# Kernel optimization log

Hardware: AMD Instinct MI355X
Metric: run time of the kernel (lower is better)

Reference implementation:

```python
import jax, jax.numpy as jnp
import numpy as np

STRIDES = {"p3": 8, "p4": 16, "p5": 32}
SHAPES = {"p3": (100, 152), "p4": (50, 76), "p5": (25, 38)}
STRIDE_SCALE = 4
ASPECT_RATIOS = (0.5, 1.0, 2.0)
SCALE_CLAMP = float(np.log(224.0 / 8.0))
TOPK = 2000


def fpn_location_coords(level):
    H, W = SHAPES[level]
    s = STRIDES[level]
    # NOTE: original code uses arange(feat_shape[2]) for x and feat_shape[3] for y,
    # with meshgrid(y_vals, x_vals); replicate exactly.
    x_vals = s * (jnp.arange(H, dtype=jnp.float32) + 0.5)
    y_vals = s * (jnp.arange(W, dtype=jnp.float32) + 0.5)
    y_grid, x_grid = jnp.meshgrid(y_vals, x_vals, indexing="ij")
    return jnp.stack([x_grid.reshape(-1), y_grid.reshape(-1)], axis=1)  # (H*W, 2)


def generate_anchors(locations, level):
    s = STRIDES[level]
    anchor_size = STRIDE_SCALE * s
    area = float(anchor_size) ** 2
    boxes = []
    for ar in ASPECT_RATIOS:
        w = (area / ar) ** 0.5
        h = area / w
        half = jnp.array([w, h], dtype=jnp.float32) * 0.5
        tl = locations - half
        br = locations + half
        boxes.append(jnp.concatenate([tl, br], axis=1))  # (HW, 4)
    boxes = jnp.stack(boxes, axis=1)  # (HW, A, 4)
    return boxes.reshape(-1, 4)


def apply_deltas(deltas, anchors):
    d = deltas
    dxy = d[:, :2]
    dwh = jnp.minimum(d[:, 2:], SCALE_CLAMP)
    centers = jnp.stack([(anchors[:, 0] + anchors[:, 2]) * 0.5,
                         (anchors[:, 1] + anchors[:, 3]) * 0.5], axis=1)
    dims = jnp.stack([anchors[:, 2] - anchors[:, 0],
                      anchors[:, 3] - anchors[:, 1]], axis=1)
    new_c = centers + dims * dxy
    new_d = dims * jnp.exp(dwh)
    return jnp.concatenate([new_c - 0.5 * new_d, new_c + 0.5 * new_d], axis=1)


def iou(b1, b2):
    # b1: (M,4), b2: (N,4) -> (M,N)
    xl = jnp.maximum(b1[:, None, 0], b2[None, :, 0])
    yl = jnp.maximum(b1[:, None, 1], b2[None, :, 1])
    xr = jnp.minimum(b1[:, None, 2], b2[None, :, 2])
    yr = jnp.minimum(b1[:, None, 3], b2[None, :, 3])
    inter = jnp.clip(xr - xl, 0.0) * jnp.clip(yr - yl, 0.0)
    a1 = (b1[:, 2] - b1[:, 0]) * (b1[:, 3] - b1[:, 1])
    a2 = (b2[:, 2] - b2[:, 0]) * (b2[:, 3] - b2[:, 1])
    return inter / (a1[:, None] + a2[None, :] - inter)


def setup_inputs() -> dict:
    key = jax.random.key(0)
    ks = jax.random.split(key, 6)
    d = {}
    d["feat_p3"] = jax.random.normal(ks[0], (1, 256, 100, 152), jnp.float32)
    d["feat_p4"] = jax.random.normal(ks[1], (1, 256, 50, 76), jnp.float32)
    d["feat_p5"] = jax.random.normal(ks[2], (1, 256, 25, 38), jnp.float32)
    d["deltas_p3"] = jax.random.normal(ks[3], (45600, 4), jnp.float32) * 0.1
    d["deltas_p4"] = jax.random.normal(ks[4], (11400, 4), jnp.float32) * 0.1
    d["deltas_p5"] = jax.random.normal(ks[5], (2850, 4), jnp.float32) * 0.1
    return d


def reference(feat_p3, feat_p4, feat_p5, deltas_p3, deltas_p4, deltas_p5):
    deltas = {"p3": deltas_p3, "p4": deltas_p4, "p5": deltas_p5}
    boxes_all = []
    anchors_all = []
    for level in ("p3", "p4", "p5"):
        locs = fpn_location_coords(level)
        anchors = generate_anchors(locs, level)
        boxes = apply_deltas(deltas[level], anchors)
        boxes_all.append(boxes)
        anchors_all.append(anchors)
    boxes = jnp.concatenate(boxes_all, axis=0)      # (59850, 4)
    anchors = jnp.concatenate(anchors_all, axis=0)  # (59850, 4)
    # proposal scoring proxy: score by box area magnitude of first TOPK slice
    proposals = boxes[:TOPK]
    ious = iou(proposals, anchors)  # (2000, 59850)
    max_iou = jnp.max(ious, axis=0)  # (59850,)
    return boxes, anchors, max_iou


if __name__ == "__main__":
    out = reference(**setup_inputs())
    print([o.shape for o in out])
```

## Files before the change

kernel.cpp:

```cpp
#include <hip/hip_runtime.h>
#include <math.h>

#define NTOT      59850
#define NPROP     2000
#define ANCH_OFF  239400
#define MIOU_OFF  478800
#define NCHUNK    32
#define CS        64
#define GXI       16
#define BUILD_PER 120

struct BuildConsts {
    float hw[3][3];
    float hh[3][3];
    float clampv;
};

__device__ __forceinline__ float4 make_box(float x, float y, float hwv, float hhv,
                                           float4 d, float clampv)
{
    float ax0 = x - hwv, ay0 = y - hhv;
    float ax1 = x + hwv, ay1 = y + hhv;
    float w  = ax1 - ax0, h = ay1 - ay0;
    float cx = (ax0 + ax1) * 0.5f, cy = (ay0 + ay1) * 0.5f;
    float dwx = fminf(d.z, clampv), dwy = fminf(d.w, clampv);
    float ncx = cx + w * d.x, ncy = cy + h * d.y;
    float nw  = w * expf(dwx), nh = h * expf(dwy);
    return make_float4(ncx - 0.5f * nw, ncy - 0.5f * nh,
                       ncx + 0.5f * nw, ncy + 0.5f * nh);
}

__device__ __forceinline__ void anchor_from_id(int g, const BuildConsts& C,
    float& x, float& y, float& hwv, float& hhv)
{
    if (g < 45600) {
        int loc = g / 3, r = g - loc * 3;
        int i = loc / 100, j = loc - i * 100;
        x = 8.f * ((float)j + 0.5f);  y = 8.f * ((float)i + 0.5f);
        hwv = C.hw[0][r]; hhv = C.hh[0][r];
    } else if (g < 57000) {
        int a = g - 45600;
        int loc = a / 3, r = a - loc * 3;
        int i = loc / 50, j = loc - i * 50;
        x = 16.f * ((float)j + 0.5f); y = 16.f * ((float)i + 0.5f);
        hwv = C.hw[1][r]; hhv = C.hh[1][r];
    } else {
        int a = g - 57000;
        int loc = a / 3, r = a - loc * 3;
        int i = loc / 25, j = loc - i * 25;
        x = 32.f * ((float)j + 0.5f); y = 32.f * ((float)i + 0.5f);
        hwv = C.hw[2][r]; hhv = C.hh[2][r];
    }
}

#define RECT(L, S, NX, NY, i0v, j0v, njv, nv)                                  \
    int i0v, j0v, njv, nv;                                                     \
    {                                                                          \
        float hwm = C.hw[L][0], hhm = C.hh[L][2];                              \
        int j0t = (int)floorf((bb.x - hwm) * (1.0f / S) - 0.5f) - 1;           \
        int j1t = (int)ceilf ((bb.z + hwm) * (1.0f / S) - 0.5f) + 1;           \
        int i0t = (int)floorf((bb.y - hhm) * (1.0f / S) - 0.5f) - 1;           \
        int i1t = (int)ceilf ((bb.w + hhm) * (1.0f / S) - 0.5f) + 1;           \
        j0t = max(0, j0t); j1t = min(NX - 1, j1t);                             \
        i0t = max(0, i0t); i1t = min(NY - 1, i1t);                             \
        int njt = j1t - j0t + 1, nit = i1t - i0t + 1;                          \
        if (njt < 0) njt = 0;                                                  \
        if (nit < 0) nit = 0;                                                  \
        i0v = i0t; j0v = j0t; njv = njt; nv = nit * njt * 3;                   \
    }

__global__ __launch_bounds__(256) void rpn_kernel(
    const float4* __restrict__ d3,
    const float4* __restrict__ d4,
    const float4* __restrict__ d5,
    float* __restrict__ out,
    BuildConsts C)
{
    __shared__ float4 Pb[CS];
    __shared__ float  Pa[CS];
    __shared__ float4 bbS;

    int tid = threadIdx.x;
    int bx  = blockIdx.x;
    int cy  = blockIdx.y;
    float* miou = out + MIOU_OFF;

    int gb = (cy * GXI + bx) * BUILD_PER + tid;
    if (tid < BUILD_PER && gb < NTOT) {
        const float4* dl; int a;
        if (gb < 45600)      { dl = d3; a = gb; }
        else if (gb < 57000) { dl = d4; a = gb - 45600; }
        else                 { dl = d5; a = gb - 57000; }
        float x, y, hwv, hhv;
        anchor_from_id(gb, C, x, y, hwv, hhv);
        ((float4*)out)[gb] = make_box(x, y, hwv, hhv, dl[a], C.clampv);
        ((float4*)(out + ANCH_OFF))[gb] =
            make_float4(x - hwv, y - hhv, x + hwv, y + hhv);
        if (((const int*)miou)[gb] < 0)
            atomicMax((int*)(miou + gb), 0);
    }

    if (tid < CS) {
        int p = cy * CS + tid;
        p = p < NPROP ? p : NPROP - 1;
        int loc = p / 3, r = p - loc * 3;
        int i = loc / 100, j = loc - i * 100;
        float x = 8.0f * ((float)j + 0.5f);
        float y = 8.0f * ((float)i + 0.5f);
        float4 b = make_box(x, y, C.hw[0][r], C.hh[0][r], d3[p], C.clampv);
        Pb[tid] = b;
        Pa[tid] = (b.z - b.x) * (b.w - b.y);
        float bx0 = b.x, by0 = b.y, bx1 = b.z, by1 = b.w;
        #pragma unroll
        for (int m = 32; m; m >>= 1) {
            bx0 = fminf(bx0, __shfl_xor(bx0, m));
            by0 = fminf(by0, __shfl_xor(by0, m));
            bx1 = fmaxf(bx1, __shfl_xor(bx1, m));
            by1 = fmaxf(by1, __shfl_xor(by1, m));
        }
        if (tid == 0) bbS = make_float4(bx0, by0, bx1, by1);
    }
    __syncthreads();
    float4 bb = bbS;

    RECT(0,  8.f, 100, 152, i0L0, j0L0, njL0, nL0)
    RECT(1, 16.f,  50,  76, i0L1, j0L1, njL1, nL1)
    RECT(2, 32.f,  25,  38, i0L2, j0L2, njL2, nL2)
    int b1 = nL0, b2 = nL0 + nL1, NL = b2 + nL2;

    for (int pos = bx * 256 + tid; pos < NL; pos += GXI * 256) {
        bool ge1 = pos >= b1, ge2 = pos >= b2;
        int t      = pos - (ge2 ? b2 : (ge1 ? b1 : 0));
        unsigned nj = (unsigned)(ge2 ? njL2 : (ge1 ? njL1 : njL0));
        int i0s    = ge2 ? i0L2 : (ge1 ? i0L1 : i0L0);
        int j0s    = ge2 ? j0L2 : (ge1 ? j0L1 : j0L0);
        float s    = ge2 ? 32.f : (ge1 ? 16.f : 8.f);
        int nx     = ge2 ? 25 : (ge1 ? 50 : 100);
        int gbase  = ge2 ? 57000 : (ge1 ? 45600 : 0);

        unsigned tu  = (unsigned)t;
        unsigned loc = tu / 3u;
        int r        = (int)(tu - loc * 3u);
        unsigned irow = loc / nj;
        unsigned jcol = loc - irow * nj;
        int i = i0s + (int)irow, j = j0s + (int)jcol;

        float x = s * ((float)j + 0.5f);
        float y = s * ((float)i + 0.5f);
        float hwA = ge2 ? C.hw[2][0] : (ge1 ? C.hw[1][0] : C.hw[0][0]);
        float hwB = ge2 ? C.hw[2][1] : (ge1 ? C.hw[1][1] : C.hw[0][1]);
        float hwC = ge2 ? C.hw[2][2] : (ge1 ? C.hw[1][2] : C.hw[0][2]);
        float hhA = ge2 ? C.hh[2][0] : (ge1 ? C.hh[1][0] : C.hh[0][0]);
        float hhB = ge2 ? C.hh[2][1] : (ge1 ? C.hh[1][1] : C.hh[0][1]);
        float hhC = ge2 ? C.hh[2][2] : (ge1 ? C.hh[1][2] : C.hh[0][2]);
        float hwv = (r == 0) ? hwA : ((r == 1) ? hwB : hwC);
        float hhv = (r == 0) ? hhA : ((r == 1) ? hhB : hhC);

        float ax0 = x - hwv, ay0 = y - hhv;
        float ax1 = x + hwv, ay1 = y + hhv;
        float a2  = (2.0f * hwv) * (2.0f * hhv);

        float Ib = 0.0f, Sb = 1.0f;
        #pragma unroll 8
        for (int p = 0; p < CS; ++p) {
            float4 b  = Pb[p];
            float  pa = Pa[p];
            float xl = fmaxf(b.x, ax0);
            float yl = fmaxf(b.y, ay0);
            float xr = fminf(b.z, ax1);
            float yr = fminf(b.w, ay1);
            float iw = fmaxf(xr - xl, 0.0f);
            float ih = fmaxf(yr - yl, 0.0f);
            float inter = iw * ih;
            float S = pa + a2;
            bool better = inter * Sb > Ib * S;
            Ib = better ? inter : Ib;
            Sb = better ? S     : Sb;
        }
        if (Ib > 0.0f) {
            float m = Ib / (Sb - Ib);
            int g = gbase + (i * nx + j) * 3 + r;
            float cur = miou[g];
            if (m > cur)
                atomicMax((int*)(miou + g), __float_as_int(m));
        }
    }
}

extern "C" void kernel_launch(void* const* d_in, const int* in_sizes, int n_in,
                              void* d_out, int out_size, void* d_ws, size_t ws_size,
                              hipStream_t stream) {
    const float4* d3 = (const float4*)d_in[3];
    const float4* d4 = (const float4*)d_in[4];
    const float4* d5 = (const float4*)d_in[5];
    float* out = (float*)d_out;

    BuildConsts C;
    const double sArr[3]  = {8.0, 16.0, 32.0};
    const double arArr[3] = {0.5, 1.0, 2.0};
    for (int l = 0; l < 3; ++l) {
        double as   = 4.0 * sArr[l];
        double area = as * as;
        for (int rr = 0; rr < 3; ++rr) {
            double w = sqrt(area / arArr[rr]);
            double h = area / w;
            C.hw[l][rr] = (float)w * 0.5f;
            C.hh[l][rr] = (float)h * 0.5f;
        }
    }
    C.clampv = (float)log(224.0 / 8.0);

    rpn_kernel<<<dim3(GXI, NCHUNK), 256, 0, stream>>>(d3, d4, d5, out, C);
}
```

Before: 19.38 us.

## Split proposal chunk across wave lanes in registers with shuffle max-reduce

Instead of each thread looping over 64 proposals held in shared memory, each wavefront now holds its chunk's 64 proposals in registers, 4 per lane across 16 lanes. Four anchors are processed per wave-iteration, and the per-anchor best IoU is combined with xor-shuffle reductions. This removes the shared-memory staging and the block-wide barrier, and spreads work over 1024 one-dimensional blocks whose waves each take a (chunk, anchor-stride) slot. The cost is extra shuffle work per anchor, only one lane in 16 issuing the atomic, and four times more proposal box construction, since every wave rebuilds its own proposals.

```diff
diff --git a/kernel.cpp b/kernel.cpp
--- a/kernel.cpp
+++ b/kernel.cpp
@@ -6,9 +6,9 @@
 #define ANCH_OFF  239400
 #define MIOU_OFF  478800
 #define NCHUNK    32
-#define CS        64
-#define GXI       16
-#define BUILD_PER 120
+#define NBLK      1024
+#define BUILD_PER 60
+#define RHO_N     128
 
 struct BuildConsts {
     float hw[3][3];
@@ -76,16 +76,11 @@
     float* __restrict__ out,
     BuildConsts C)
 {
-    __shared__ float4 Pb[CS];
-    __shared__ float  Pa[CS];
-    __shared__ float4 bbS;
-
     int tid = threadIdx.x;
-    int bx  = blockIdx.x;
-    int cy  = blockIdx.y;
+    int bid = blockIdx.x;
     float* miou = out + MIOU_OFF;
 
-    int gb = (cy * GXI + bx) * BUILD_PER + tid;
+    int gb = bid * BUILD_PER + tid;
     if (tid < BUILD_PER && gb < NTOT) {
         const float4* dl; int a;
         if (gb < 45600)      { dl = d3; a = gb; }
@@ -100,37 +95,60 @@
             atomicMax((int*)(miou + gb), 0);
     }
 
-    if (tid < CS) {
-        int p = cy * CS + tid;
-        p = p < NPROP ? p : NPROP - 1;
-        int loc = p / 3, r = p - loc * 3;
-        int i = loc / 100, j = loc - i * 100;
-        float x = 8.0f * ((float)j + 0.5f);
-        float y = 8.0f * ((float)i + 0.5f);
-        float4 b = make_box(x, y, C.hw[0][r], C.hh[0][r], d3[p], C.clampv);
-        Pb[tid] = b;
-        Pa[tid] = (b.z - b.x) * (b.w - b.y);
-        float bx0 = b.x, by0 = b.y, bx1 = b.z, by1 = b.w;
-        #pragma unroll
-        for (int m = 32; m; m >>= 1) {
-            bx0 = fminf(bx0, __shfl_xor(bx0, m));
-            by0 = fminf(by0, __shfl_xor(by0, m));
-            bx1 = fmaxf(bx1, __shfl_xor(bx1, m));
-            by1 = fmaxf(by1, __shfl_xor(by1, m));
-        }
-        if (tid == 0) bbS = make_float4(bx0, by0, bx1, by1);
-    }
-    __syncthreads();
-    float4 bb = bbS;
+    int wid  = (bid << 2) | (tid >> 6);
+    int cy   = wid & (NCHUNK - 1);
+    int rho  = wid >> 5;
+    int lane = tid & 63;
+    int grp  = lane >> 4;
+    int sub  = lane & 15;
+
+    float4 B0, B1, B2, B3;
+    float  A0, A1, A2v, A3;
+    {
+        int pb = cy * 64 + sub;
+#define MKP(K, BV, AV)                                                         \
+        {                                                                      \
+            int p = pb + 16 * K;                                               \
+            p = p < NPROP ? p : NPROP - 1;           \
+            int loc = p / 3, r = p - loc * 3;                                  \
+            int ii = loc / 100, jj = loc - ii * 100;                           \
+            float x = 8.0f * ((float)jj + 0.5f);                               \
+            float y = 8.0f * ((float)ii + 0.5f);                               \
+            BV = make_box(x, y, C.hw[0][r], C.hh[0][r], d3[p], C.clampv);      \
+            AV = (BV.z - BV.x) * (BV.w - BV.y);                                \
+        }
+        MKP(0, B0, A0)
+        MKP(1, B1, A1)
+        MKP(2, B2, A2v)
+        MKP(3, B3, A3)
+#undef MKP
+    }
+
+    float bx0 = fminf(fminf(B0.x, B1.x), fminf(B2.x, B3.x));
+    float by0 = fminf(fminf(B0.y, B1.y), fminf(B2.y, B3.y));
+    float bx1 = fmaxf(fmaxf(B0.z, B1.z), fmaxf(B2.z, B3.z));
+    float by1 = fmaxf(fmaxf(B0.w, B1.w), fmaxf(B2.w, B3.w));
+    #pragma unroll
+    for (int m = 1; m < 64; m <<= 1) {
+        bx0 = fminf(bx0, __shfl_xor(bx0, m));
+        by0 = fminf(by0, __shfl_xor(by0, m));
+        bx1 = fmaxf(bx1, __shfl_xor(bx1, m));
+        by1 = fmaxf(by1, __shfl_xor(by1, m));
+    }
+    float4 bb = make_float4(bx0, by0, bx1, by1);
 
     RECT(0,  8.f, 100, 152, i0L0, j0L0, njL0, nL0)
     RECT(1, 16.f,  50,  76, i0L1, j0L1, njL1, nL1)
     RECT(2, 32.f,  25,  38, i0L2, j0L2, njL2, nL2)
     int b1 = nL0, b2 = nL0 + nL1, NL = b2 + nL2;
 
-    for (int pos = bx * 256 + tid; pos < NL; pos += GXI * 256) {
-        bool ge1 = pos >= b1, ge2 = pos >= b2;
-        int t      = pos - (ge2 ? b2 : (ge1 ? b1 : 0));
+    for (int sg = rho; sg * 4 < NL; sg += RHO_N) {
+        int pos  = sg * 4 + grp;
+        bool vld = pos < NL;
+        int cpos = vld ? pos : 0;
+
+        bool ge1 = cpos >= b1, ge2 = cpos >= b2;
+        int t      = cpos - (ge2 ? b2 : (ge1 ? b1 : 0));
         unsigned nj = (unsigned)(ge2 ? njL2 : (ge1 ? njL1 : njL0));
         int i0s    = ge2 ? i0L2 : (ge1 ? i0L1 : i0L0);
         int j0s    = ge2 ? j0L2 : (ge1 ? j0L1 : j0L0);
@@ -138,9 +156,9 @@
         int nx     = ge2 ? 25 : (ge1 ? 50 : 100);
         int gbase  = ge2 ? 57000 : (ge1 ? 45600 : 0);
 
-        unsigned tu  = (unsigned)t;
-        unsigned loc = tu / 3u;
-        int r        = (int)(tu - loc * 3u);
+        unsigned tu   = (unsigned)t;
+        unsigned loc  = tu / 3u;
+        int r         = (int)(tu - loc * 3u);
         unsigned irow = loc / nj;
         unsigned jcol = loc - irow * nj;
         int i = i0s + (int)irow, j = j0s + (int)jcol;
@@ -161,28 +179,37 @@
         float a2  = (2.0f * hwv) * (2.0f * hhv);
 
         float Ib = 0.0f, Sb = 1.0f;
-        #pragma unroll 8
-        for (int p = 0; p < CS; ++p) {
-            float4 b  = Pb[p];
-            float  pa = Pa[p];
-            float xl = fmaxf(b.x, ax0);
-            float yl = fmaxf(b.y, ay0);
-            float xr = fminf(b.z, ax1);
-            float yr = fminf(b.w, ay1);
-            float iw = fmaxf(xr - xl, 0.0f);
-            float ih = fmaxf(yr - yl, 0.0f);
-            float inter = iw * ih;
-            float S = pa + a2;
-            bool better = inter * Sb > Ib * S;
-            Ib = better ? inter : Ib;
-            Sb = better ? S     : Sb;
-        }
-        if (Ib > 0.0f) {
-            float m = Ib / (Sb - Ib);
+#define PAIR(BV, AV)                                                           \
+        {                                                                      \
+            float xl = fmaxf(BV.x, ax0), yl = fmaxf(BV.y, ay0);                \
+            float xr = fminf(BV.z, ax1), yr = fminf(BV.w, ay1);                \
+            float iw = fmaxf(xr - xl, 0.0f);                                   \
+            float ih = fmaxf(yr - yl, 0.0f);                                   \
+            float inter = iw * ih;                                             \
+            float S = AV + a2;                                                 \
+            bool bt = inter * Sb > Ib * S;    \
+            Ib = bt ? inter : Ib; Sb = bt ? S : Sb;                            \
+        }
+        PAIR(B0, A0)
+        PAIR(B1, A1)
+        PAIR(B2, A2v)
+        PAIR(B3, A3)
+#undef PAIR
+
+        #pragma unroll
+        for (int m = 1; m < 16; m <<= 1) {
+            float I2 = __shfl_xor(Ib, m);
+            float S2 = __shfl_xor(Sb, m);
+            bool bt = I2 * Sb > Ib * S2;
+            Ib = bt ? I2 : Ib; Sb = bt ? S2 : Sb;
+        }
+
+        if (sub == 0 && vld && Ib > 0.0f) {
+            float mv = Ib / (Sb - Ib);
             int g = gbase + (i * nx + j) * 3 + r;
             float cur = miou[g];
-            if (m > cur)
-                atomicMax((int*)(miou + g), __float_as_int(m));
+            if (mv > cur)
+                atomicMax((int*)(miou + g), __float_as_int(mv));
         }
     }
 }
@@ -210,5 +237,5 @@
     }
     C.clampv = (float)log(224.0 / 8.0);
 
-    rpn_kernel<<<dim3(GXI, NCHUNK), 256, 0, stream>>>(d3, d4, d5, out, C);
-}
+    rpn_kernel<<<dim3(NBLK), 256, 0, stream>>>(d3, d4, d5, out, C);
+}
```

After: 22.36 us. 1.15x slower.

## Widen grid to 64 x-blocks and split IoU max loop into two accumulators

Applied to the files above, without the earlier changes.

Raises the number of x-blocks per proposal chunk from 16 to 64 and shrinks per-block build work to match, so the launch has four times as many blocks and fills more compute units. It also adds an occupancy hint to launch bounds. The inner best-IoU reduction is split into two independent accumulator chains over the two halves of the proposal chunk, merged at the end, to shorten the dependent compare/select chain. The trade-off is more per-block fixed work: every block still builds its proposal tile and bounding rectangle, which is now repeated across more blocks.

```diff
diff --git a/kernel.cpp b/kernel.cpp
--- a/kernel.cpp
+++ b/kernel.cpp
@@ -7,8 +7,8 @@
 #define MIOU_OFF  478800
 #define NCHUNK    32
 #define CS        64
-#define GXI       16
-#define BUILD_PER 120
+#define GXI       64
+#define BUILD_PER 30
 
 struct BuildConsts {
     float hw[3][3];
@@ -69,7 +69,7 @@
         i0v = i0t; j0v = j0t; njv = njt; nv = nit * njt * 3;                   \
     }
 
-__global__ __launch_bounds__(256) void rpn_kernel(
+__global__ __launch_bounds__(256, 8) void rpn_kernel(
     const float4* __restrict__ d3,
     const float4* __restrict__ d4,
     const float4* __restrict__ d5,
@@ -160,23 +160,36 @@
         float ax1 = x + hwv, ay1 = y + hhv;
         float a2  = (2.0f * hwv) * (2.0f * hhv);
 
-        float Ib = 0.0f, Sb = 1.0f;
-        #pragma unroll 8
-        for (int p = 0; p < CS; ++p) {
-            float4 b  = Pb[p];
-            float  pa = Pa[p];
-            float xl = fmaxf(b.x, ax0);
-            float yl = fmaxf(b.y, ay0);
-            float xr = fminf(b.z, ax1);
-            float yr = fminf(b.w, ay1);
-            float iw = fmaxf(xr - xl, 0.0f);
-            float ih = fmaxf(yr - yl, 0.0f);
-            float inter = iw * ih;
-            float S = pa + a2;
-            bool better = inter * Sb > Ib * S;
-            Ib = better ? inter : Ib;
-            Sb = better ? S     : Sb;
-        }
+        float Ib0 = 0.0f, Sb0 = 1.0f;
+        float Ib1 = 0.0f, Sb1 = 1.0f;
+        #pragma unroll 4
+        for (int p = 0; p < 32; ++p) {
+            {
+                float4 b  = Pb[p];
+                float  pa = Pa[p];
+                float xl = fmaxf(b.x, ax0), yl = fmaxf(b.y, ay0);
+                float xr = fminf(b.z, ax1), yr = fminf(b.w, ay1);
+                float iw = fmaxf(xr - xl, 0.0f), ih = fmaxf(yr - yl, 0.0f);
+                float inter = iw * ih;
+                float S = pa + a2;
+                bool bt = inter * Sb0 > Ib0 * S;
+                Ib0 = bt ? inter : Ib0; Sb0 = bt ? S : Sb0;
+            }
+            {
+                float4 b  = Pb[p + 32];
+                float  pa = Pa[p + 32];
+                float xl = fmaxf(b.x, ax0), yl = fmaxf(b.y, ay0);
+                float xr = fminf(b.z, ax1), yr = fminf(b.w, ay1);
+                float iw = fmaxf(xr - xl, 0.0f), ih = fmaxf(yr - yl, 0.0f);
+                float inter = iw * ih;
+                float S = pa + a2;
+                bool bt = inter * Sb1 > Ib1 * S;
+                Ib1 = bt ? inter : Ib1; Sb1 = bt ? S : Sb1;
+            }
+        }
+        bool mt = Ib1 * Sb0 > Ib0 * Sb1;
+        float Ib = mt ? Ib1 : Ib0, Sb = mt ? Sb1 : Sb0;
+
         if (Ib > 0.0f) {
             float m = Ib / (Sb - Ib);
             int g = gbase + (i * nx + j) * 3 + r;
```

After: 36.08 us. +86.2%, slower.
